# Performance work log

Hardware: AMD Instinct MI355X
Metric: run time of the kernel (lower is better)

## Reference

```python
import jax, jax.numpy as jnp
import numpy as np

B, N, F_IN, F_OUT = 8, 2048, 256, 64
ALPHA = 0.2          # LeakyReLU negative slope
NEG_INF = -9e15      # matches -9000000000000000.0 in the torch code


def setup_inputs() -> dict:
    key = jax.random.key(0)
    k = jax.random.split(key, 7)
    x = jax.random.normal(k[0], (B, N, F_IN), dtype=jnp.float32)
    adj = jax.random.randint(k[1], (B, N, N), 0, 2, dtype=jnp.int32)
    # W: nn.Linear(in_features, out_features)
    W = jax.random.normal(k[2], (F_IN, F_OUT), dtype=jnp.float32) / np.sqrt(F_IN)
    b_W = jax.random.normal(k[3], (F_OUT,), dtype=jnp.float32) * 0.01
    # a: nn.Linear(2*out_features, 1); decomposed as a_src (first F_OUT rows,
    # multiplies h_i) and a_dst (last F_OUT rows, multiplies h_j) + bias.
    a_src = jax.random.normal(k[4], (F_OUT,), dtype=jnp.float32) / np.sqrt(2 * F_OUT)
    a_dst = jax.random.normal(k[5], (F_OUT,), dtype=jnp.float32) / np.sqrt(2 * F_OUT)
    a_b = jax.random.normal(k[6], (), dtype=jnp.float32) * 0.01
    return {"x": x, "adj": adj, "W": W, "b_W": b_W,
            "a_src": a_src, "a_dst": a_dst, "a_b": a_b}


def reference(x, adj, W, b_W, a_src, a_dst, a_b):
    # h = W(input): [B, N, F_OUT]
    h = jnp.einsum('bnf,fo->bno', x, W) + b_W
    # Additive attention decomposition: a([h_i || h_j]) = a_src.h_i + a_dst.h_j + b
    # (avoids materializing the [B, N, N, 2F] concat tensor of the original)
    src = jnp.einsum('bno,o->bn', h, a_src)  # row term  (h_i)
    dst = jnp.einsum('bno,o->bn', h, a_dst)  # col term  (h_j)
    e = jax.nn.leaky_relu(src[:, :, None] + dst[:, None, :] + a_b, ALPHA)  # [B,N,N]
    e = jnp.where(adj > 0, e, NEG_INF)
    attention = jax.nn.softmax(e, axis=2)
    h_prime = jnp.einsum('bij,bjo->bio', attention, h)  # [B, N, F_OUT]
    return jax.nn.elu(h_prime)  # concat=True branch
```

## Files before the change

kernel.cpp:

```cpp
#include <hip/hip_runtime.h>

#define B_   8
#define N_   2048
#define FIN  256
#define FOUT 64
#define ALPHA 0.2f

typedef __attribute__((ext_vector_type(8))) short bf16x8;
typedef __attribute__((ext_vector_type(8))) unsigned short u16x8;
typedef __attribute__((ext_vector_type(4))) float f32x4;

__device__ __forceinline__ float b2f(unsigned short u) {
    union { unsigned int u; float f; } v; v.u = ((unsigned int)u) << 16; return v.f;
}
__device__ __forceinline__ unsigned short f2b(float f) {
    union { float f; unsigned int u; } v; v.f = f;
    unsigned int r = v.u + 0x7FFFu + ((v.u >> 16) & 1u);
    return (unsigned short)(r >> 16);
}

__global__ __launch_bounds__(256) void k_hgemm_tr(
    const float* __restrict__ x, const float* __restrict__ W,
    const float* __restrict__ bW, const float* __restrict__ asrc,
    const float* __restrict__ adst,
    unsigned short* __restrict__ hT, float* __restrict__ src, float* __restrict__ dst)
{
    __shared__ unsigned short tileT[FOUT * 72];
    __shared__ float as_s[FOUT], ad_s[FOUT];

    const int tid = threadIdx.x;
    const int wv = tid >> 6, lane = tid & 63;
    const int quad = lane >> 4, col = lane & 15;
    const int f = wv * 16 + col;

    if (tid < FOUT) { as_s[tid] = asrc[tid]; ad_s[tid] = adst[tid]; }

    bf16x8 Bf[8];
    #pragma unroll
    for (int kk = 0; kk < 8; ++kk) {
        bf16x8 t;
        #pragma unroll
        for (int j = 0; j < 8; ++j)
            t[j] = (short)f2b(W[(kk * 32 + quad * 8 + j) * FOUT + f]);
        Bf[kk] = t;
    }
    const float bias = bW[f];
    const int r0 = blockIdx.x * 64;
    const int b = r0 >> 11;
    const int j0b = r0 & (N_ - 1);

    #pragma unroll
    for (int rt = 0; rt < 4; ++rt) {
        const int rr = r0 + rt * 16;
        f32x4 acc = {0.f, 0.f, 0.f, 0.f};
        #pragma unroll
        for (int kk = 0; kk < 8; ++kk) {
            const float* xp = x + (size_t)(rr + col) * FIN + kk * 32 + quad * 8;
            float4 x0 = *(const float4*)xp;
            float4 x1 = *(const float4*)(xp + 4);
            bf16x8 Af;
            Af[0] = (short)f2b(x0.x); Af[1] = (short)f2b(x0.y);
            Af[2] = (short)f2b(x0.z); Af[3] = (short)f2b(x0.w);
            Af[4] = (short)f2b(x1.x); Af[5] = (short)f2b(x1.y);
            Af[6] = (short)f2b(x1.z); Af[7] = (short)f2b(x1.w);
            acc = __builtin_amdgcn_mfma_f32_16x16x32_bf16(Af, Bf[kk], acc, 0, 0, 0);
        }
        #pragma unroll
        for (int reg = 0; reg < 4; ++reg) {
            int row = rt * 16 + quad * 4 + reg;
            tileT[f * 72 + row] = f2b(acc[reg] + bias);
        }
    }
    __syncthreads();

    {
        const int i = tid >> 2, fb = (tid & 3) * 16;
        float sp = 0.f, dp = 0.f;
        #pragma unroll
        for (int k = 0; k < 16; ++k) {
            float hv = b2f(tileT[(fb + k) * 72 + i]);
            sp += hv * as_s[fb + k]; dp += hv * ad_s[fb + k];
        }
        sp += __shfl_xor(sp, 1); sp += __shfl_xor(sp, 2);
        dp += __shfl_xor(dp, 1); dp += __shfl_xor(dp, 2);
        if ((tid & 3) == 0) { src[r0 + i] = sp; dst[r0 + i] = dp; }
    }
    {
        const int fq = tid >> 2, ic = (tid & 3) * 16;
        u16x8 o0 = *(const u16x8*)&tileT[fq * 72 + ic];
        u16x8 o1 = *(const u16x8*)&tileT[fq * 72 + ic + 8];
        unsigned short* op = hT + (size_t)(b * FOUT + fq) * N_ + j0b + ic;
        *(u16x8*)op = o0;
        *(u16x8*)(op + 8) = o1;
    }
}

__global__ __launch_bounds__(256) void k_attn(
    const int* __restrict__ adj, const float* __restrict__ src, const float* __restrict__ dst,
    const unsigned short* __restrict__ hT, const float* __restrict__ abp,
    float* __restrict__ out)
{
    __shared__ unsigned short h_s[2][64 * 136];
    __shared__ unsigned short w_s[2][32 * 136];
    __shared__ float src_s[32];
    __shared__ float l_s[32];

    const int tid = threadIdx.x;
    const int wv = tid >> 6, lane = tid & 63;
    const int quad = lane >> 4, col = lane & 15;
    const int b = blockIdx.x >> 6;
    const int i0 = (blockIdx.x & 63) * 32;

    if (tid < 32) src_s[tid] = src[b * N_ + i0 + tid];
    __syncthreads();

    const int il = tid >> 3, jg = tid & 7;
    const float srci = src_s[il] + abp[0];
    const int fq = tid >> 2, q4 = tid & 3;
    const unsigned short* hTbase = hT + (size_t)(b * FOUT + fq) * N_ + q4 * 32;
    const int* adjbase = adj + (size_t)(b * N_ + i0 + il) * N_ + jg * 16;
    const float* dstbase = dst + b * N_ + jg * 16;

    u16x8 hv0 = *(const u16x8*)(hTbase);
    u16x8 hv1 = *(const u16x8*)(hTbase + 8);
    u16x8 hv2 = *(const u16x8*)(hTbase + 16);
    u16x8 hv3 = *(const u16x8*)(hTbase + 24);
    int4 a0 = *(const int4*)(adjbase);
    int4 a1 = *(const int4*)(adjbase + 4);
    int4 a2 = *(const int4*)(adjbase + 8);
    int4 a3 = *(const int4*)(adjbase + 12);
    float4 d0 = *(const float4*)(dstbase);
    float4 d1 = *(const float4*)(dstbase + 4);
    float4 d2 = *(const float4*)(dstbase + 8);
    float4 d3 = *(const float4*)(dstbase + 12);

    float lsum = 0.f;
    f32x4 acc0 = {0, 0, 0, 0}, acc1 = {0, 0, 0, 0};

    for (int jt = 0; jt < 16; ++jt) {
        const int buf = jt & 1;
        {
            unsigned short* q = &h_s[buf][fq * 136 + q4 * 32];
            *(u16x8*)q = hv0; *(u16x8*)(q + 8) = hv1;
            *(u16x8*)(q + 16) = hv2; *(u16x8*)(q + 24) = hv3;
        }
        {
            int av[16] = {a0.x, a0.y, a0.z, a0.w, a1.x, a1.y, a1.z, a1.w,
                          a2.x, a2.y, a2.z, a2.w, a3.x, a3.y, a3.z, a3.w};
            float dv[16] = {d0.x, d0.y, d0.z, d0.w, d1.x, d1.y, d1.z, d1.w,
                            d2.x, d2.y, d2.z, d2.w, d3.x, d3.y, d3.z, d3.w};
            u16x8 p0, p1;
            float ls = 0.f;
            #pragma unroll
            for (int k = 0; k < 16; ++k) {
                float e = srci + dv[k];
                e = e > 0.f ? e : ALPHA * e;
                float wval = av[k] > 0 ? __expf(e) : 0.f;
                unsigned short wb = f2b(wval);
                ls += b2f(wb);
                if (k < 8) p0[k] = wb; else p1[k - 8] = wb;
            }
            lsum += ls;
            unsigned short* q = &w_s[buf][il * 136 + jg * 16];
            *(u16x8*)q = p0; *(u16x8*)(q + 8) = p1;
        }
        __syncthreads();
        {
            const int jn = ((jt + 1) & 15) * 128;
            hv0 = *(const u16x8*)(hTbase + jn);
            hv1 = *(const u16x8*)(hTbase + jn + 8);
            hv2 = *(const u16x8*)(hTbase + jn + 16);
            hv3 = *(const u16x8*)(hTbase + jn + 24);
            a0 = *(const int4*)(adjbase + jn);
            a1 = *(const int4*)(adjbase + jn + 4);
            a2 = *(const int4*)(adjbase + jn + 8);
            a3 = *(const int4*)(adjbase + jn + 12);
            d0 = *(const float4*)(dstbase + jn);
            d1 = *(const float4*)(dstbase + jn + 4);
            d2 = *(const float4*)(dstbase + jn + 8);
            d3 = *(const float4*)(dstbase + jn + 12);
        }
        {
            #pragma unroll
            for (int kk = 0; kk < 4; ++kk) {
                bf16x8 A0 = *(const bf16x8*)&w_s[buf][col * 136 + kk * 32 + quad * 8];
                bf16x8 A1 = *(const bf16x8*)&w_s[buf][(16 + col) * 136 + kk * 32 + quad * 8];
                bf16x8 Bf = *(const bf16x8*)&h_s[buf][(wv * 16 + col) * 136 + kk * 32 + quad * 8];
                acc0 = __builtin_amdgcn_mfma_f32_16x16x32_bf16(A0, Bf, acc0, 0, 0, 0);
                acc1 = __builtin_amdgcn_mfma_f32_16x16x32_bf16(A1, Bf, acc1, 0, 0, 0);
            }
        }
    }

    lsum += __shfl_xor(lsum, 1);
    lsum += __shfl_xor(lsum, 2);
    lsum += __shfl_xor(lsum, 4);
    if (jg == 0) l_s[il] = lsum;
    __syncthreads();

    #pragma unroll
    for (int m = 0; m < 2; ++m) {
        f32x4 a = m ? acc1 : acc0;
        #pragma unroll
        for (int reg = 0; reg < 4; ++reg) {
            int row = m * 16 + quad * 4 + reg;
            float l = l_s[row];
            l = l > 0.f ? l : 1.f;
            float v = a[reg] / l;
            v = v > 0.f ? v : (__expf(v) - 1.f);
            out[(size_t)(b * N_ + i0 + row) * FOUT + wv * 16 + col] = v;
        }
    }
}

extern "C" void kernel_launch(void* const* d_in, const int* in_sizes, int n_in,
                              void* d_out, int out_size, void* d_ws, size_t ws_size,
                              hipStream_t stream)
{
    const float* x    = (const float*)d_in[0];
    const int*   adj  = (const int*)d_in[1];
    const float* W    = (const float*)d_in[2];
    const float* bW   = (const float*)d_in[3];
    const float* asrc = (const float*)d_in[4];
    const float* adst = (const float*)d_in[5];
    const float* abp  = (const float*)d_in[6];
    float* out = (float*)d_out;

    char* ws = (char*)d_ws;
    unsigned short* hT = (unsigned short*)ws;
    float* src = (float*)(ws + (size_t)2 * 1024 * 1024);
    float* dst = (float*)(ws + (size_t)2 * 1024 * 1024 + 64 * 1024);

    k_hgemm_tr<<<256, 256, 0, stream>>>(x, W, bW, asrc, adst, hT, src, dst);
    k_attn<<<512, 256, 0, stream>>>(adj, src, dst, hT, abp, out);
}
```

Before: 220.8 us.

## Load attention B-operand directly from global, prefetch two tiles ahead, shrink GEMM blocks

The attention kernel no longer stages hT through shared memory. Each wave loads its MFMA B fragments straight from global memory into registers, with double-buffered register sets. Adjacency and dst loads are now issued two tiles ahead, and the full __syncthreads is replaced by an lgkmcnt wait plus s_barrier, which cuts LDS traffic and barrier stalls. The projection GEMM kernel now processes 16 rows per block across 4x as many blocks for more parallelism, at the cost of narrower hT stores and more register pressure.

```diff
diff --git a/kernel.cpp b/kernel.cpp
--- a/kernel.cpp
+++ b/kernel.cpp
@@ -8,6 +8,7 @@
 
 typedef __attribute__((ext_vector_type(8))) short bf16x8;
 typedef __attribute__((ext_vector_type(8))) unsigned short u16x8;
+typedef __attribute__((ext_vector_type(4))) unsigned short u16x4;
 typedef __attribute__((ext_vector_type(4))) float f32x4;
 
 __device__ __forceinline__ float b2f(unsigned short u) {
@@ -25,7 +26,7 @@
     const float* __restrict__ adst,
     unsigned short* __restrict__ hT, float* __restrict__ src, float* __restrict__ dst)
 {
-    __shared__ unsigned short tileT[FOUT * 72];
+    __shared__ unsigned short tileT[FOUT * 20];
     __shared__ float as_s[FOUT], ad_s[FOUT];
 
     const int tid = threadIdx.x;
@@ -45,54 +46,93 @@
         Bf[kk] = t;
     }
     const float bias = bW[f];
-    const int r0 = blockIdx.x * 64;
+    const int r0 = blockIdx.x * 16;
     const int b = r0 >> 11;
     const int j0b = r0 & (N_ - 1);
 
-    #pragma unroll
-    for (int rt = 0; rt < 4; ++rt) {
-        const int rr = r0 + rt * 16;
-        f32x4 acc = {0.f, 0.f, 0.f, 0.f};
-        #pragma unroll
-        for (int kk = 0; kk < 8; ++kk) {
-            const float* xp = x + (size_t)(rr + col) * FIN + kk * 32 + quad * 8;
-            float4 x0 = *(const float4*)xp;
-            float4 x1 = *(const float4*)(xp + 4);
-            bf16x8 Af;
-            Af[0] = (short)f2b(x0.x); Af[1] = (short)f2b(x0.y);
-            Af[2] = (short)f2b(x0.z); Af[3] = (short)f2b(x0.w);
-            Af[4] = (short)f2b(x1.x); Af[5] = (short)f2b(x1.y);
-            Af[6] = (short)f2b(x1.z); Af[7] = (short)f2b(x1.w);
-            acc = __builtin_amdgcn_mfma_f32_16x16x32_bf16(Af, Bf[kk], acc, 0, 0, 0);
-        }
-        #pragma unroll
-        for (int reg = 0; reg < 4; ++reg) {
-            int row = rt * 16 + quad * 4 + reg;
-            tileT[f * 72 + row] = f2b(acc[reg] + bias);
-        }
-    }
+    f32x4 acc = {0.f, 0.f, 0.f, 0.f};
+    #pragma unroll
+    for (int kk = 0; kk < 8; ++kk) {
+        const float* xp = x + (size_t)(r0 + col) * FIN + kk * 32 + quad * 8;
+        float4 x0 = *(const float4*)xp;
+        float4 x1 = *(const float4*)(xp + 4);
+        bf16x8 Af;
+        Af[0] = (short)f2b(x0.x); Af[1] = (short)f2b(x0.y);
+        Af[2] = (short)f2b(x0.z); Af[3] = (short)f2b(x0.w);
+        Af[4] = (short)f2b(x1.x); Af[5] = (short)f2b(x1.y);
+        Af[6] = (short)f2b(x1.z); Af[7] = (short)f2b(x1.w);
+        acc = __builtin_amdgcn_mfma_f32_16x16x32_bf16(Af, Bf[kk], acc, 0, 0, 0);
+    }
+    #pragma unroll
+    for (int reg = 0; reg < 4; ++reg)
+        tileT[f * 20 + quad * 4 + reg] = f2b(acc[reg] + bias);
     __syncthreads();
 
     {
-        const int i = tid >> 2, fb = (tid & 3) * 16;
+        const int i = tid >> 4, fb = (tid & 15) * 4;
         float sp = 0.f, dp = 0.f;
         #pragma unroll
-        for (int k = 0; k < 16; ++k) {
-            float hv = b2f(tileT[(fb + k) * 72 + i]);
+        for (int k = 0; k < 4; ++k) {
+            float hv = b2f(tileT[(fb + k) * 20 + i]);
             sp += hv * as_s[fb + k]; dp += hv * ad_s[fb + k];
         }
         sp += __shfl_xor(sp, 1); sp += __shfl_xor(sp, 2);
+        sp += __shfl_xor(sp, 4); sp += __shfl_xor(sp, 8);
         dp += __shfl_xor(dp, 1); dp += __shfl_xor(dp, 2);
-        if ((tid & 3) == 0) { src[r0 + i] = sp; dst[r0 + i] = dp; }
+        dp += __shfl_xor(dp, 4); dp += __shfl_xor(dp, 8);
+        if ((tid & 15) == 0) { src[r0 + i] = sp; dst[r0 + i] = dp; }
     }
     {
-        const int fq = tid >> 2, ic = (tid & 3) * 16;
-        u16x8 o0 = *(const u16x8*)&tileT[fq * 72 + ic];
-        u16x8 o1 = *(const u16x8*)&tileT[fq * 72 + ic + 8];
+        const int fq = tid >> 2, ic = (tid & 3) * 4;
         unsigned short* op = hT + (size_t)(b * FOUT + fq) * N_ + j0b + ic;
-        *(u16x8*)op = o0;
-        *(u16x8*)(op + 8) = o1;
-    }
+        *(u16x4*)op = *(const u16x4*)&tileT[fq * 20 + ic];
+    }
+}
+
+#define ATT_TILE(Aa,Ab,Ac,Ad, Da,Db,Dc,Dd, BfC, BfN, BUF, JT)                          \
+{                                                                                      \
+    const int av[16] = {Aa.x,Aa.y,Aa.z,Aa.w, Ab.x,Ab.y,Ab.z,Ab.w,                      \
+                        Ac.x,Ac.y,Ac.z,Ac.w, Ad.x,Ad.y,Ad.z,Ad.w};                     \
+    const float dv[16] = {Da.x,Da.y,Da.z,Da.w, Db.x,Db.y,Db.z,Db.w,                    \
+                          Dc.x,Dc.y,Dc.z,Dc.w, Dd.x,Dd.y,Dd.z,Dd.w};                   \
+    u16x8 p0, p1; float ls = 0.f;                                                      \
+    _Pragma("unroll")                                                                  \
+    for (int k = 0; k < 16; ++k) {                                                     \
+        float e = srci + dv[k];                                                        \
+        e = e > 0.f ? e : ALPHA * e;                                                   \
+        float wval = av[k] > 0 ? __expf(e) : 0.f;                                      \
+        unsigned short wb = f2b(wval);                                                 \
+        ls += b2f(wb);         \
+        if (k < 8) p0[k] = wb; else p1[k - 8] = wb;                                    \
+    }                                                                                  \
+    lsum += ls;                                                                        \
+    {   unsigned short* q = &w_s[BUF][il * 136 + jg * 16];                             \
+        *(u16x8*)q = p0; *(u16x8*)(q + 8) = p1; }                                      \
+    {                  \
+        const int jn = (((JT) + 2) & 15) * 128;                                        \
+        Aa = *(const int4*)(adjbase + jn);                                             \
+        Ab = *(const int4*)(adjbase + jn + 4);                                         \
+        Ac = *(const int4*)(adjbase + jn + 8);                                         \
+        Ad = *(const int4*)(adjbase + jn + 12);                                        \
+        Da = *(const float4*)(dstbase + jn);                                           \
+        Db = *(const float4*)(dstbase + jn + 4);                                       \
+        Dc = *(const float4*)(dstbase + jn + 8);                                       \
+        Dd = *(const float4*)(dstbase + jn + 12); }                                    \
+                  \
+    asm volatile("s_waitcnt lgkmcnt(0)\n\ts_barrier" ::: "memory");                    \
+    {                        \
+        const int jn = (((JT) + 1) & 15) * 128;                                        \
+        BfN[0] = *(const bf16x8*)(hfbase + jn);                                        \
+        BfN[1] = *(const bf16x8*)(hfbase + jn + 32);                                   \
+        BfN[2] = *(const bf16x8*)(hfbase + jn + 64);                                   \
+        BfN[3] = *(const bf16x8*)(hfbase + jn + 96); }                                 \
+    _Pragma("unroll")                                                                  \
+    for (int kk = 0; kk < 4; ++kk) {                                                   \
+        bf16x8 A0 = *(const bf16x8*)&w_s[BUF][col * 136 + kk * 32 + quad * 8];         \
+        bf16x8 A1 = *(const bf16x8*)&w_s[BUF][(16 + col) * 136 + kk * 32 + quad * 8];  \
+        acc0 = __builtin_amdgcn_mfma_f32_16x16x32_bf16(A0, BfC[kk], acc0, 0, 0, 0);    \
+        acc1 = __builtin_amdgcn_mfma_f32_16x16x32_bf16(A1, BfC[kk], acc1, 0, 0, 0);    \
+    }                                                                                  \
 }
 
 __global__ __launch_bounds__(256) void k_attn(
@@ -100,7 +140,6 @@
     const unsigned short* __restrict__ hT, const float* __restrict__ abp,
     float* __restrict__ out)
 {
-    __shared__ unsigned short h_s[2][64 * 136];
     __shared__ unsigned short w_s[2][32 * 136];
     __shared__ float src_s[32];
     __shared__ float l_s[32];
@@ -116,80 +155,39 @@
 
     const int il = tid >> 3, jg = tid & 7;
     const float srci = src_s[il] + abp[0];
-    const int fq = tid >> 2, q4 = tid & 3;
-    const unsigned short* hTbase = hT + (size_t)(b * FOUT + fq) * N_ + q4 * 32;
     const int* adjbase = adj + (size_t)(b * N_ + i0 + il) * N_ + jg * 16;
     const float* dstbase = dst + b * N_ + jg * 16;
-
-    u16x8 hv0 = *(const u16x8*)(hTbase);
-    u16x8 hv1 = *(const u16x8*)(hTbase + 8);
-    u16x8 hv2 = *(const u16x8*)(hTbase + 16);
-    u16x8 hv3 = *(const u16x8*)(hTbase + 24);
+    const unsigned short* hfbase = hT + (size_t)(b * FOUT + wv * 16 + col) * N_ + quad * 8;
+
     int4 a0 = *(const int4*)(adjbase);
     int4 a1 = *(const int4*)(adjbase + 4);
     int4 a2 = *(const int4*)(adjbase + 8);
     int4 a3 = *(const int4*)(adjbase + 12);
+    int4 a4 = *(const int4*)(adjbase + 128);
+    int4 a5 = *(const int4*)(adjbase + 132);
+    int4 a6 = *(const int4*)(adjbase + 136);
+    int4 a7 = *(const int4*)(adjbase + 140);
     float4 d0 = *(const float4*)(dstbase);
     float4 d1 = *(const float4*)(dstbase + 4);
     float4 d2 = *(const float4*)(dstbase + 8);
     float4 d3 = *(const float4*)(dstbase + 12);
+    float4 d4 = *(const float4*)(dstbase + 128);
+    float4 d5 = *(const float4*)(dstbase + 132);
+    float4 d6 = *(const float4*)(dstbase + 136);
+    float4 d7 = *(const float4*)(dstbase + 140);
+    bf16x8 bfE[4], bfO[4];
+    bfE[0] = *(const bf16x8*)(hfbase);
+    bfE[1] = *(const bf16x8*)(hfbase + 32);
+    bfE[2] = *(const bf16x8*)(hfbase + 64);
+    bfE[3] = *(const bf16x8*)(hfbase + 96);
 
     float lsum = 0.f;
     f32x4 acc0 = {0, 0, 0, 0}, acc1 = {0, 0, 0, 0};
 
-    for (int jt = 0; jt < 16; ++jt) {
-        const int buf = jt & 1;
-        {
-            unsigned short* q = &h_s[buf][fq * 136 + q4 * 32];
-            *(u16x8*)q = hv0; *(u16x8*)(q + 8) = hv1;
-            *(u16x8*)(q + 16) = hv2; *(u16x8*)(q + 24) = hv3;
-        }
-        {
-            int av[16] = {a0.x, a0.y, a0.z, a0.w, a1.x, a1.y, a1.z, a1.w,
-                          a2.x, a2.y, a2.z, a2.w, a3.x, a3.y, a3.z, a3.w};
-            float dv[16] = {d0.x, d0.y, d0.z, d0.w, d1.x, d1.y, d1.z, d1.w,
-                            d2.x, d2.y, d2.z, d2.w, d3.x, d3.y, d3.z, d3.w};
-            u16x8 p0, p1;
-            float ls = 0.f;
-            #pragma unroll
-            for (int k = 0; k < 16; ++k) {
-                float e = srci + dv[k];
-                e = e > 0.f ? e : ALPHA * e;
-                float wval = av[k] > 0 ? __expf(e) : 0.f;
-                unsigned short wb = f2b(wval);
-                ls += b2f(wb);
-                if (k < 8) p0[k] = wb; else p1[k - 8] = wb;
-            }
-            lsum += ls;
-            unsigned short* q = &w_s[buf][il * 136 + jg * 16];
-            *(u16x8*)q = p0; *(u16x8*)(q + 8) = p1;
-        }
-        __syncthreads();
-        {
-            const int jn = ((jt + 1) & 15) * 128;
-            hv0 = *(const u16x8*)(hTbase + jn);
-            hv1 = *(const u16x8*)(hTbase + jn + 8);
-            hv2 = *(const u16x8*)(hTbase + jn + 16);
-            hv3 = *(const u16x8*)(hTbase + jn + 24);
-            a0 = *(const int4*)(adjbase + jn);
-            a1 = *(const int4*)(adjbase + jn + 4);
-            a2 = *(const int4*)(adjbase + jn + 8);
-            a3 = *(const int4*)(adjbase + jn + 12);
-            d0 = *(const float4*)(dstbase + jn);
-            d1 = *(const float4*)(dstbase + jn + 4);
-            d2 = *(const float4*)(dstbase + jn + 8);
-            d3 = *(const float4*)(dstbase + jn + 12);
-        }
-        {
-            #pragma unroll
-            for (int kk = 0; kk < 4; ++kk) {
-                bf16x8 A0 = *(const bf16x8*)&w_s[buf][col * 136 + kk * 32 + quad * 8];
-                bf16x8 A1 = *(const bf16x8*)&w_s[buf][(16 + col) * 136 + kk * 32 + quad * 8];
-                bf16x8 Bf = *(const bf16x8*)&h_s[buf][(wv * 16 + col) * 136 + kk * 32 + quad * 8];
-                acc0 = __builtin_amdgcn_mfma_f32_16x16x32_bf16(A0, Bf, acc0, 0, 0, 0);
-                acc1 = __builtin_amdgcn_mfma_f32_16x16x32_bf16(A1, Bf, acc1, 0, 0, 0);
-            }
-        }
+    for (int it = 0; it < 8; ++it) {
+        const int jt = it * 2;
+        ATT_TILE(a0, a1, a2, a3, d0, d1, d2, d3, bfE, bfO, 0, jt)
+        ATT_TILE(a4, a5, a6, a7, d4, d5, d6, d7, bfO, bfE, 1, jt + 1)
     }
 
     lsum += __shfl_xor(lsum, 1);
@@ -231,6 +229,6 @@
     float* src = (float*)(ws + (size_t)2 * 1024 * 1024);
     float* dst = (float*)(ws + (size_t)2 * 1024 * 1024 + 64 * 1024);
 
-    k_hgemm_tr<<<256, 256, 0, stream>>>(x, W, bW, asrc, adst, hT, src, dst);
+    k_hgemm_tr<<<1024, 256, 0, stream>>>(x, W, bW, asrc, adst, hT, src, dst);
     k_attn<<<512, 256, 0, stream>>>(adj, src, dst, hT, abp, out);
 }
```

After: 223.1 us. No clear change (+1.0%).

## Shrink attention row tile to 16, load h fragments directly, pack bf16 in hardware

Applied to the files above, without the earlier changes.

The attention kernel now handles 16 rows per block with 1024 blocks. Each wave reads its h B-fragments straight from global memory into registers, so the shared-memory staging of h goes away. The exp weights are packed with v_cvt_pk_bf16_f32, and the loop is unrolled two tiles at a time with explicit even/odd register sets and a raw lgkmcnt wait plus barrier. This cuts LDS traffic and increases the number of blocks for the bandwidth-bound adj stream, at the cost of re-reading h from global/L2 once per 16 rows instead of per 32.

```diff
diff --git a/kernel.cpp b/kernel.cpp
--- a/kernel.cpp
+++ b/kernel.cpp
@@ -95,121 +95,114 @@
     }
 }
 
+#define TILE(AC0,AC1, DC0,DC1, HC0,HC1,HC2,HC3, AN0,AN1, DN0,DN1, HN0,HN1,HN2,HN3, BUF, T) \
+{                                                                                      \
+    const int av[8] = {AC0.x,AC0.y,AC0.z,AC0.w, AC1.x,AC1.y,AC1.z,AC1.w};              \
+    const float dv[8] = {DC0.x,DC0.y,DC0.z,DC0.w, DC1.x,DC1.y,DC1.z,DC1.w};            \
+    int4 pkv; float ls = 0.f;                                                          \
+    _Pragma("unroll")                                                                  \
+    for (int p = 0; p < 4; ++p) {                                                      \
+        float e0 = srci + dv[2 * p];                                                   \
+        float e1 = srci + dv[2 * p + 1];                                               \
+        e0 = fmaxf(e0, ALPHA * e0);            \
+        e1 = fmaxf(e1, ALPHA * e1);                                                    \
+        float w0 = av[2 * p]     > 0 ? __expf(e0) : 0.f;                               \
+        float w1 = av[2 * p + 1] > 0 ? __expf(e1) : 0.f;                               \
+        unsigned int r;                                                                \
+        asm("v_cvt_pk_bf16_f32 %0, %1, %2" : "=v"(r) : "v"(w0), "v"(w1));              \
+        ((unsigned int*)&pkv)[p] = r;                                                  \
+        union { unsigned int u; float f; } lo, hi;                                     \
+        lo.u = r << 16; hi.u = r & 0xFFFF0000u;                                        \
+        ls += lo.f + hi.f;        \
+    }                                                                                  \
+    lsum += ls;                                                                        \
+    *(int4*)&w_s[BUF][il * 136 + jg * 8] = pkv;                                        \
+    {                          \
+        const int jn = (((T) + 1) & 15) * 128;                                         \
+        AN0 = *(const int4*)(adjp + jn);                                               \
+        AN1 = *(const int4*)(adjp + jn + 4);                                           \
+        DN0 = *(const float4*)(dstp + jn);                                             \
+        DN1 = *(const float4*)(dstp + jn + 4); }                                       \
+                            \
+    asm volatile("s_waitcnt lgkmcnt(0)\n\ts_barrier" ::: "memory");                    \
+    {                       \
+        const int jn = (((T) + 1) & 15) * 128;                                         \
+        HN0 = *(const bf16x8*)(hfp + jn);                                              \
+        HN1 = *(const bf16x8*)(hfp + jn + 32);                                         \
+        HN2 = *(const bf16x8*)(hfp + jn + 64);                                         \
+        HN3 = *(const bf16x8*)(hfp + jn + 96); }                                       \
+    {                         \
+        bf16x8 A0;                                                                     \
+        A0 = *(const bf16x8*)&w_s[BUF][col * 136 + 0 * 32 + quad * 8];                 \
+        acc = __builtin_amdgcn_mfma_f32_16x16x32_bf16(A0, HC0, acc, 0, 0, 0);          \
+        A0 = *(const bf16x8*)&w_s[BUF][col * 136 + 1 * 32 + quad * 8];                 \
+        acc = __builtin_amdgcn_mfma_f32_16x16x32_bf16(A0, HC1, acc, 0, 0, 0);          \
+        A0 = *(const bf16x8*)&w_s[BUF][col * 136 + 2 * 32 + quad * 8];                 \
+        acc = __builtin_amdgcn_mfma_f32_16x16x32_bf16(A0, HC2, acc, 0, 0, 0);          \
+        A0 = *(const bf16x8*)&w_s[BUF][col * 136 + 3 * 32 + quad * 8];                 \
+        acc = __builtin_amdgcn_mfma_f32_16x16x32_bf16(A0, HC3, acc, 0, 0, 0);          \
+    }                                                                                  \
+}
+
 __global__ __launch_bounds__(256) void k_attn(
-    const int* __restrict__ adj, const float* __restrict__ src, const float* __restrict__ dst,
-    const unsigned short* __restrict__ hT, const float* __restrict__ abp,
-    float* __restrict__ out)
+    const int* __restrict__ adj, const float* __restrict__ src,
+    const float* __restrict__ dst, const unsigned short* __restrict__ hT,
+    const float* __restrict__ abp, float* __restrict__ out)
 {
-    __shared__ unsigned short h_s[2][64 * 136];
-    __shared__ unsigned short w_s[2][32 * 136];
-    __shared__ float src_s[32];
-    __shared__ float l_s[32];
+    __shared__ unsigned short w_s[2][16 * 136];
+    __shared__ float src_s[16];
+    __shared__ float l_s[16];
 
     const int tid = threadIdx.x;
     const int wv = tid >> 6, lane = tid & 63;
     const int quad = lane >> 4, col = lane & 15;
-    const int b = blockIdx.x >> 6;
-    const int i0 = (blockIdx.x & 63) * 32;
-
-    if (tid < 32) src_s[tid] = src[b * N_ + i0 + tid];
+    const int gr0 = blockIdx.x * 16;
+    const int b = gr0 >> 11;
+
+    if (tid < 16) src_s[tid] = src[gr0 + tid];
     __syncthreads();
 
-    const int il = tid >> 3, jg = tid & 7;
+    const int il = tid >> 4, jg = tid & 15;
     const float srci = src_s[il] + abp[0];
-    const int fq = tid >> 2, q4 = tid & 3;
-    const unsigned short* hTbase = hT + (size_t)(b * FOUT + fq) * N_ + q4 * 32;
-    const int* adjbase = adj + (size_t)(b * N_ + i0 + il) * N_ + jg * 16;
-    const float* dstbase = dst + b * N_ + jg * 16;
-
-    u16x8 hv0 = *(const u16x8*)(hTbase);
-    u16x8 hv1 = *(const u16x8*)(hTbase + 8);
-    u16x8 hv2 = *(const u16x8*)(hTbase + 16);
-    u16x8 hv3 = *(const u16x8*)(hTbase + 24);
-    int4 a0 = *(const int4*)(adjbase);
-    int4 a1 = *(const int4*)(adjbase + 4);
-    int4 a2 = *(const int4*)(adjbase + 8);
-    int4 a3 = *(const int4*)(adjbase + 12);
-    float4 d0 = *(const float4*)(dstbase);
-    float4 d1 = *(const float4*)(dstbase + 4);
-    float4 d2 = *(const float4*)(dstbase + 8);
-    float4 d3 = *(const float4*)(dstbase + 12);
+    const int* adjp = adj + (size_t)(gr0 + il) * N_ + jg * 8;
+    const float* dstp = dst + b * N_ + jg * 8;
+    const unsigned short* hfp = hT + ((size_t)b * FOUT + wv * 16 + col) * N_ + quad * 8;
+
+    int4 aE0 = *(const int4*)(adjp);
+    int4 aE1 = *(const int4*)(adjp + 4);
+    float4 dE0 = *(const float4*)(dstp);
+    float4 dE1 = *(const float4*)(dstp + 4);
+    bf16x8 hE0 = *(const bf16x8*)(hfp);
+    bf16x8 hE1 = *(const bf16x8*)(hfp + 32);
+    bf16x8 hE2 = *(const bf16x8*)(hfp + 64);
+    bf16x8 hE3 = *(const bf16x8*)(hfp + 96);
+    int4 aO0, aO1; float4 dO0, dO1; bf16x8 hO0, hO1, hO2, hO3;
 
     float lsum = 0.f;
-    f32x4 acc0 = {0, 0, 0, 0}, acc1 = {0, 0, 0, 0};
-
-    for (int jt = 0; jt < 16; ++jt) {
-        const int buf = jt & 1;
-        {
-            unsigned short* q = &h_s[buf][fq * 136 + q4 * 32];
-            *(u16x8*)q = hv0; *(u16x8*)(q + 8) = hv1;
-            *(u16x8*)(q + 16) = hv2; *(u16x8*)(q + 24) = hv3;
-        }
-        {
-            int av[16] = {a0.x, a0.y, a0.z, a0.w, a1.x, a1.y, a1.z, a1.w,
-                          a2.x, a2.y, a2.z, a2.w, a3.x, a3.y, a3.z, a3.w};
-            float dv[16] = {d0.x, d0.y, d0.z, d0.w, d1.x, d1.y, d1.z, d1.w,
-                            d2.x, d2.y, d2.z, d2.w, d3.x, d3.y, d3.z, d3.w};
-            u16x8 p0, p1;
-            float ls = 0.f;
-            #pragma unroll
-            for (int k = 0; k < 16; ++k) {
-                float e = srci + dv[k];
-                e = e > 0.f ? e : ALPHA * e;
-                float wval = av[k] > 0 ? __expf(e) : 0.f;
-                unsigned short wb = f2b(wval);
-                ls += b2f(wb);
-                if (k < 8) p0[k] = wb; else p1[k - 8] = wb;
-            }
-            lsum += ls;
-            unsigned short* q = &w_s[buf][il * 136 + jg * 16];
-            *(u16x8*)q = p0; *(u16x8*)(q + 8) = p1;
-        }
-        __syncthreads();
-        {
-            const int jn = ((jt + 1) & 15) * 128;
-            hv0 = *(const u16x8*)(hTbase + jn);
-            hv1 = *(const u16x8*)(hTbase + jn + 8);
-            hv2 = *(const u16x8*)(hTbase + jn + 16);
-            hv3 = *(const u16x8*)(hTbase + jn + 24);
-            a0 = *(const int4*)(adjbase + jn);
-            a1 = *(const int4*)(adjbase + jn + 4);
-            a2 = *(const int4*)(adjbase + jn + 8);
-            a3 = *(const int4*)(adjbase + jn + 12);
-            d0 = *(const float4*)(dstbase + jn);
-            d1 = *(const float4*)(dstbase + jn + 4);
-            d2 = *(const float4*)(dstbase + jn + 8);
-            d3 = *(const float4*)(dstbase + jn + 12);
-        }
-        {
-            #pragma unroll
-            for (int kk = 0; kk < 4; ++kk) {
-                bf16x8 A0 = *(const bf16x8*)&w_s[buf][col * 136 + kk * 32 + quad * 8];
-                bf16x8 A1 = *(const bf16x8*)&w_s[buf][(16 + col) * 136 + kk * 32 + quad * 8];
-                bf16x8 Bf = *(const bf16x8*)&h_s[buf][(wv * 16 + col) * 136 + kk * 32 + quad * 8];
-                acc0 = __builtin_amdgcn_mfma_f32_16x16x32_bf16(A0, Bf, acc0, 0, 0, 0);
-                acc1 = __builtin_amdgcn_mfma_f32_16x16x32_bf16(A1, Bf, acc1, 0, 0, 0);
-            }
-        }
+    f32x4 acc = {0, 0, 0, 0};
+
+    for (int t = 0; t < 16; t += 2) {
+        TILE(aE0, aE1, dE0, dE1, hE0, hE1, hE2, hE3,
+             aO0, aO1, dO0, dO1, hO0, hO1, hO2, hO3, 0, t)
+        TILE(aO0, aO1, dO0, dO1, hO0, hO1, hO2, hO3,
+             aE0, aE1, dE0, dE1, hE0, hE1, hE2, hE3, 1, t + 1)
     }
 
     lsum += __shfl_xor(lsum, 1);
     lsum += __shfl_xor(lsum, 2);
     lsum += __shfl_xor(lsum, 4);
+    lsum += __shfl_xor(lsum, 8);
     if (jg == 0) l_s[il] = lsum;
     __syncthreads();
 
     #pragma unroll
-    for (int m = 0; m < 2; ++m) {
-        f32x4 a = m ? acc1 : acc0;
-        #pragma unroll
-        for (int reg = 0; reg < 4; ++reg) {
-            int row = m * 16 + quad * 4 + reg;
-            float l = l_s[row];
-            l = l > 0.f ? l : 1.f;
-            float v = a[reg] / l;
-            v = v > 0.f ? v : (__expf(v) - 1.f);
-            out[(size_t)(b * N_ + i0 + row) * FOUT + wv * 16 + col] = v;
-        }
+    for (int reg = 0; reg < 4; ++reg) {
+        const int row = quad * 4 + reg;
+        float l = l_s[row];
+        l = l > 0.f ? l : 1.f;
+        float v = acc[reg] / l;
+        v = v > 0.f ? v : (__expf(v) - 1.f);
+        out[(size_t)(gr0 + row) * FOUT + wv * 16 + col] = v;
     }
 }
 
@@ -232,5 +225,5 @@
     float* dst = (float*)(ws + (size_t)2 * 1024 * 1024 + 64 * 1024);
 
     k_hgemm_tr<<<256, 256, 0, stream>>>(x, W, bW, asrc, adst, hT, src, dst);
-    k_attn<<<512, 256, 0, stream>>>(adj, src, dst, hT, abp, out);
-}
+    k_attn<<<1024, 256, 0, stream>>>(adj, src, dst, hT, abp, out);
+}
```

New measurement: 224.6 us. No clear change (+1.7%).

## Split attention key dimension across two blocks and add a reduction kernel

Applied to the files above, without the earlier changes.

Each attention block now handles half of the j (neighbor) range, which doubles the grid from 512 to 1024 blocks. Partial numerators and softmax denominators go to workspace, and a new reduce kernel sums the two halves, normalizes and applies ELU. The goal is more parallelism and better coverage of the CUs for a kernel bound by streaming adj. The cost is an extra launch and a write and read of the partial buffers, about 8MB each way.

```diff
diff --git a/kernel.cpp b/kernel.cpp
--- a/kernel.cpp
+++ b/kernel.cpp
@@ -98,18 +98,20 @@
 __global__ __launch_bounds__(256) void k_attn(
     const int* __restrict__ adj, const float* __restrict__ src, const float* __restrict__ dst,
     const unsigned short* __restrict__ hT, const float* __restrict__ abp,
-    float* __restrict__ out)
+    float* __restrict__ pnum, float* __restrict__ pden)
 {
     __shared__ unsigned short h_s[2][64 * 136];
     __shared__ unsigned short w_s[2][32 * 136];
     __shared__ float src_s[32];
-    __shared__ float l_s[32];
 
     const int tid = threadIdx.x;
     const int wv = tid >> 6, lane = tid & 63;
     const int quad = lane >> 4, col = lane & 15;
-    const int b = blockIdx.x >> 6;
-    const int i0 = (blockIdx.x & 63) * 32;
+    const int g = blockIdx.x >> 1;
+    const int half = blockIdx.x & 1;
+    const int b = g >> 6;
+    const int i0 = (g & 63) * 32;
+    const int j0 = half << 10;
 
     if (tid < 32) src_s[tid] = src[b * N_ + i0 + tid];
     __syncthreads();
@@ -117,9 +119,9 @@
     const int il = tid >> 3, jg = tid & 7;
     const float srci = src_s[il] + abp[0];
     const int fq = tid >> 2, q4 = tid & 3;
-    const unsigned short* hTbase = hT + (size_t)(b * FOUT + fq) * N_ + q4 * 32;
-    const int* adjbase = adj + (size_t)(b * N_ + i0 + il) * N_ + jg * 16;
-    const float* dstbase = dst + b * N_ + jg * 16;
+    const unsigned short* hTbase = hT + (size_t)(b * FOUT + fq) * N_ + j0 + q4 * 32;
+    const int* adjbase = adj + (size_t)(b * N_ + i0 + il) * N_ + j0 + jg * 16;
+    const float* dstbase = dst + b * N_ + j0 + jg * 16;
 
     u16x8 hv0 = *(const u16x8*)(hTbase);
     u16x8 hv1 = *(const u16x8*)(hTbase + 8);
@@ -137,7 +139,7 @@
     float lsum = 0.f;
     f32x4 acc0 = {0, 0, 0, 0}, acc1 = {0, 0, 0, 0};
 
-    for (int jt = 0; jt < 16; ++jt) {
+    for (int jt = 0; jt < 8; ++jt) {
         const int buf = jt & 1;
         {
             unsigned short* q = &h_s[buf][fq * 136 + q4 * 32];
@@ -166,7 +168,7 @@
         }
         __syncthreads();
         {
-            const int jn = ((jt + 1) & 15) * 128;
+            const int jn = ((jt + 1) & 7) * 128;
             hv0 = *(const u16x8*)(hTbase + jn);
             hv1 = *(const u16x8*)(hTbase + jn + 8);
             hv2 = *(const u16x8*)(hTbase + jn + 16);
@@ -195,22 +197,37 @@
     lsum += __shfl_xor(lsum, 1);
     lsum += __shfl_xor(lsum, 2);
     lsum += __shfl_xor(lsum, 4);
-    if (jg == 0) l_s[il] = lsum;
-    __syncthreads();
-
+    if (jg == 0) pden[((size_t)half << 14) + g * 32 + il] = lsum;
+
+    float* pb = pnum + ((size_t)half << 20) + (size_t)g * 2048 + wv * 16 + col;
     #pragma unroll
     for (int m = 0; m < 2; ++m) {
         f32x4 a = m ? acc1 : acc0;
         #pragma unroll
-        for (int reg = 0; reg < 4; ++reg) {
-            int row = m * 16 + quad * 4 + reg;
-            float l = l_s[row];
-            l = l > 0.f ? l : 1.f;
-            float v = a[reg] / l;
-            v = v > 0.f ? v : (__expf(v) - 1.f);
-            out[(size_t)(b * N_ + i0 + row) * FOUT + wv * 16 + col] = v;
-        }
-    }
+        for (int reg = 0; reg < 4; ++reg)
+            pb[(m * 16 + quad * 4 + reg) * 64] = a[reg];
+    }
+}
+
+__global__ __launch_bounds__(256) void k_reduce(
+    const float* __restrict__ pnum, const float* __restrict__ pden,
+    float* __restrict__ out)
+{
+    const int idx = blockIdx.x * 256 + threadIdx.x;
+    const int r = idx >> 4;
+    const size_t e = (size_t)idx * 4;
+    const float4 n0 = *(const float4*)&pnum[e];
+    const float4 n1 = *(const float4*)&pnum[(1u << 20) + e];
+    float den = pden[r] + pden[(1 << 14) + r];
+    den = den > 0.f ? den : 1.f;
+    float4 v;
+    v.x = (n0.x + n1.x) / den; v.y = (n0.y + n1.y) / den;
+    v.z = (n0.z + n1.z) / den; v.w = (n0.w + n1.w) / den;
+    v.x = v.x > 0.f ? v.x : (__expf(v.x) - 1.f);
+    v.y = v.y > 0.f ? v.y : (__expf(v.y) - 1.f);
+    v.z = v.z > 0.f ? v.z : (__expf(v.z) - 1.f);
+    v.w = v.w > 0.f ? v.w : (__expf(v.w) - 1.f);
+    *(float4*)&out[e] = v;
 }
 
 extern "C" void kernel_launch(void* const* d_in, const int* in_sizes, int n_in,
@@ -228,9 +245,12 @@
 
     char* ws = (char*)d_ws;
     unsigned short* hT = (unsigned short*)ws;
-    float* src = (float*)(ws + (size_t)2 * 1024 * 1024);
-    float* dst = (float*)(ws + (size_t)2 * 1024 * 1024 + 64 * 1024);
+    float* src  = (float*)(ws + (size_t)2 * 1024 * 1024);
+    float* dst  = (float*)(ws + (size_t)2 * 1024 * 1024 + 64 * 1024);
+    float* pnum = (float*)(ws + (size_t)4 * 1024 * 1024);
+    float* pden = (float*)(ws + (size_t)16 * 1024 * 1024);
 
     k_hgemm_tr<<<256, 256, 0, stream>>>(x, W, bW, asrc, adst, hT, src, dst);
-    k_attn<<<512, 256, 0, stream>>>(adj, src, dst, hT, abp, out);
-}
+    k_attn<<<1024, 256, 0, stream>>>(adj, src, dst, hT, abp, pnum, pden);
+    k_reduce<<<1024, 256, 0, stream>>>(pnum, pden, out);
+}
```

Result: slower. 227.5 us (+3.0%).
